# Performance work log

Measured on AMD Instinct MI355X. Metric: run time of the kernel, lower is better.

Reference implementation:

```python
import jax, jax.numpy as jnp
import numpy as np

N = 2048          # num agents / graph nodes
D = 128           # n_actor == n_map
ALPHA = 0.2       # GAT leakyrelu alpha
NEG = -1e9
X_IDX = [4, 9, 14, 19]   # actors_inter_cat time indices per LSTM step
E_IDX = [0, 4, 9, 14]    # graph_adjs time indices per LSTM step


def setup_inputs() -> dict:
    key = jax.random.key(0)
    ks = jax.random.split(key, 10)
    xavier = lambda k, shape: jax.random.uniform(
        k, shape, jnp.float32, -1.0, 1.0) * 1.414 * np.sqrt(6.0 / (shape[-2] + shape[-1]))
    actors_inter_cat = jax.random.normal(ks[0], (N, 20, D), jnp.float32)
    graph_adjs = jax.random.randint(ks[1], (N, 20, N), 0, 2, jnp.int32)
    # 4 GAT_SRF gates (forget, input, input_cell, output), stacked on leading axis
    Wg = xavier(ks[2], (4, 2 * D, D))          # gate projection W: in=2*D, out=D
    ag = xavier(ks[3], (4, 2 * D))             # attention vector a (2*out_features,)
    W = xavier(ks[4], (D, D))                  # GAT cell output projection
    b = xavier(ks[5], (1, D))
    h0 = xavier(ks[6], (1, D))
    conv_w = jax.random.normal(ks[7], (3, D, D, 2), jnp.float32) * (1.0 / np.sqrt(2 * D))
    conv_b = jax.random.normal(ks[8], (3, D), jnp.float32) * 0.01
    return {"actors_inter_cat": actors_inter_cat, "graph_adjs": graph_adjs,
            "Wg": Wg, "ag": ag, "W": W, "b": b, "h0": h0,
            "conv_w": conv_w, "conv_b": conv_b}


def _gat_gates(gin, mask, Wg, ag):
    # gin: (N, 2D); mask: (N, N) bool. Computes all 4 GAT_SRF gates at once.
    Wh = jnp.einsum('nf,gfo->gno', gin, Wg)                 # (4, N, D)
    s_src = jnp.einsum('gno,go->gn', Wh, ag[:, :D])         # a^T [Wh_i ..]
    s_dst = jnp.einsum('gno,go->gn', Wh, ag[:, D:])
    e = jax.nn.leaky_relu(s_src[:, :, None] + s_dst[:, None, :], ALPHA)  # (4,N,N)
    e = jnp.where(mask[None], e, NEG)
    attn = jax.nn.softmax(e, axis=-1)
    return jax.nn.elu(jnp.einsum('gnm,gmo->gno', attn, Wh))  # concat=True -> ELU


def reference(actors_inter_cat, graph_adjs, Wg, ag, W, b, h0, conv_w, conv_b):
    n = actors_inter_cat.shape[0]
    cell = actors_inter_cat[:, 0, :]
    hidden = jnp.broadcast_to(h0, (n, D))
    outs = []
    for t in range(4):  # fixed 4-step recurrence
        X = actors_inter_cat[:, X_IDX[t], :]
        mask = graph_adjs[:, E_IDX[t], :] > 0
        gin = jnp.concatenate([X, hidden], axis=1)          # (N, 2D)
        g = _gat_gates(gin, mask, Wg, ag)                   # (4, N, D)
        forget = jax.nn.sigmoid(g[0])
        inp_gate = jax.nn.sigmoid(g[1])
        inp_cell = jnp.tanh(g[2])
        out_gate = jax.nn.sigmoid(g[3])
        cell = cell * forget + inp_gate * inp_cell
        hidden = jnp.tanh(cell) * out_gate
        outs.append(jax.nn.sigmoid(hidden @ W + b))
    y = jnp.stack(outs, axis=2)                             # (N, D, 4)
    for l in range(3):  # kernel-2 Conv1d stack: length 4 -> 3 -> 2 -> 1
        y = (jnp.einsum('nct,oc->not', y[:, :, :-1], conv_w[l, :, :, 0])
             + jnp.einsum('nct,oc->not', y[:, :, 1:], conv_w[l, :, :, 1])
             + conv_b[l][None, :, None])
    return y[:, :, 0]                                       # squeeze -> (N, D)
```

## Files before the change

kernel.cpp:

```cpp
#include <hip/hip_runtime.h>

typedef __attribute__((ext_vector_type(8))) short short8;
typedef __attribute__((ext_vector_type(4))) float floatx4;

#define MFMA16(a,b,c) __builtin_amdgcn_mfma_f32_16x16x32_bf16(a,b,c,0,0,0)

__device__ __forceinline__ unsigned short f2bf(float f){
  unsigned u = __float_as_uint(f);
  u += 0x7fffu + ((u >> 16) & 1u);
  return (unsigned short)(u >> 16);
}
__device__ __forceinline__ float sigm(float x){ return 1.f/(1.f+__expf(-x)); }


__global__ __launch_bounds__(256) void prep_kernel(const float* __restrict__ actors,
    const float* __restrict__ Wg, const float* __restrict__ W, const float* __restrict__ cw,
    const int* __restrict__ adj, float* __restrict__ cell, unsigned short* __restrict__ WgA,
    unsigned short* __restrict__ WoA, float* __restrict__ cwT,
    unsigned long long* __restrict__ bm){
  int bid = blockIdx.x;
  if (bid < 1024){
    int idx = bid*256 + threadIdx.x;
    int n = idx >> 7, c = idx & 127;
    cell[idx] = actors[(size_t)n*2560 + c];
  } else if (bid < 1536){
    int e = (bid-1024)*256 + threadIdx.x;
    int g = e >> 15, o = (e >> 8) & 127, k = e & 255;
    unsigned short v = f2bf(Wg[(size_t)g*32768 + k*128 + o]);
    int off = ((o>>4)*8 + (k>>5))*512 + (((k>>3)&3)*16 + (o&15))*8 + (k&7);
    WgA[(size_t)g*32768 + off] = v;
  } else if (bid < 1728){
    int e = (bid-1536)*256 + threadIdx.x;
    int l = e >> 14, rr = e & 16383, k = rr >> 7, o = rr & 127;
    cwT[(size_t)l*32768 + k*256 + o]       = cw[(size_t)l*32768 + o*256 + k*2];
    cwT[(size_t)l*32768 + k*256 + 128 + o] = cw[(size_t)l*32768 + o*256 + k*2 + 1];
  } else if (bid < 1792){
    int e = (bid-1728)*256 + threadIdx.x;
    int k = e >> 7, o = e & 127;
    unsigned short v = f2bf(W[(size_t)k*128 + o]);
    int off = ((o>>4)*4 + (k>>5))*512 + (((k>>3)&3)*16 + (o&15))*8 + (k&7);
    WoA[off] = v;
  } else {
    const int E[4] = {0,4,9,14};
    int mb = bid - 1792;
    int t = mb & 3, nblk = mb >> 2;
    int wv = threadIdx.x >> 6, lane = threadIdx.x & 63;
    int n = nblk*4 + wv;
    const int* row = adj + (size_t)n*40960 + (size_t)E[t]*2048;
    unsigned long long* outp = bm + ((size_t)t*2048 + n)*32;
    for (int it=0; it<32; ++it){
      unsigned long long bal = __ballot(row[it*64 + lane] > 0);
      if (lane == 0) outp[it] = bal;
    }
  }
}

__global__ __launch_bounds__(512,2) void gatewh_kernel(const float* __restrict__ actors,
    const float* __restrict__ gbuf, float* __restrict__ cell, const float* __restrict__ h0,
    const float* __restrict__ bvec, const unsigned short* __restrict__ WgA,
    const unsigned short* __restrict__ WoA, const float* __restrict__ ag,
    float* __restrict__ y, unsigned short* __restrict__ WhB,
    float* __restrict__ spart, int xoff, int t){
  __shared__ float hl[16][132];
  __shared__ __align__(16) unsigned short ginb[16*264];
  __shared__ float sredS[4][4][16], sredD[4][4][16];
  int bx = blockIdx.x;
  int tile = bx >> 1, ohalf = bx & 1;
  int n0 = tile*16, tid = threadIdx.x;
  int row = tid>>5, q = tid&31;
  {
    int o0 = q*4;
    if (t == 0){
      *(float4*)&hl[row][o0] = *(const float4*)(h0 + o0);
    } else {
      size_t idx = (size_t)(n0+row)*128 + o0;
      float4 ga = *(const float4*)(gbuf+idx);
      float4 gb = *(const float4*)(gbuf+262144+idx);
      float4 gc = *(const float4*)(gbuf+524288+idx);
      float4 gd = *(const float4*)(gbuf+786432+idx);
      float4 cv = *(const float4*)(cell+idx);
      float fg[4]={ga.x,ga.y,ga.z,ga.w}, ig[4]={gb.x,gb.y,gb.z,gb.w};
      float ic[4]={gc.x,gc.y,gc.z,gc.w}, og[4]={gd.x,gd.y,gd.z,gd.w};
      float cc[4]={cv.x,cv.y,cv.z,cv.w};
      float clv[4];
      #pragma unroll
      for (int j=0;j<4;++j){
        clv[j] = cc[j]*sigm(fg[j]) + sigm(ig[j])*tanhf(ic[j]);
        hl[row][o0+j] = tanhf(clv[j])*sigm(og[j]);
      }
      if (ohalf == 0)
        *(float4*)(cell+idx) = (float4){clv[0],clv[1],clv[2],clv[3]};
    }
  }
  __syncthreads();
  if (q < 16){
    const float* ap = actors + (size_t)(n0+row)*2560 + xoff + q*8;
    float4 a = *(const float4*)ap, bb = *(const float4*)(ap+4);
    unsigned short tmp[8] = {f2bf(a.x),f2bf(a.y),f2bf(a.z),f2bf(a.w),
                             f2bf(bb.x),f2bf(bb.y),f2bf(bb.z),f2bf(bb.w)};
    *(uint4*)&ginb[row*264 + q*8] = *(const uint4*)tmp;
  } else {
    int c0 = (q-16)*8;
    unsigned short tmp[8];
    #pragma unroll
    for (int j=0;j<8;++j) tmp[j] = f2bf(hl[row][c0+j]);
    *(uint4*)&ginb[row*264 + 128 + c0] = *(const uint4*)tmp;
  }
  __syncthreads();
  int w = tid>>6, lane = tid&63, quad = lane>>4, l16 = lane&15;
  int m32 = tile>>1, min32 = (tile&1)*16 + l16;
  int qp = min32>>3, jp = min32&7;
  if (t >= 1 && w < 4){
    int o16 = ohalf*4 + w;
    floatx4 acc = {0.f,0.f,0.f,0.f};
    #pragma unroll
    for (int kh=0; kh<4; ++kh){
      short8 bfr = *(const short8*)&ginb[l16*264 + 128 + kh*32 + quad*8];
      short8 a0 = *(const short8*)(WoA + (size_t)((o16*4 + kh)*64 + lane)*8);
      acc = MFMA16(a0, bfr, acc);
    }
    int oc = o16*16 + quad*4;
    float4 bb = *(const float4*)(bvec + oc);
    float4 res = {sigm(acc[0]+bb.x), sigm(acc[1]+bb.y),
                  sigm(acc[2]+bb.z), sigm(acc[3]+bb.w)};
    *(float4*)(y + (size_t)(t-1)*262144 + (size_t)(n0+l16)*128 + oc) = res;
  }
  #pragma unroll
  for (int ci=0; ci<2; ++ci){
    int cidx = w*2 + ci;
    int g = cidx>>2, o16q = cidx&3, o16 = ohalf*4 + o16q;
    floatx4 acc = {0.f,0.f,0.f,0.f};
    const unsigned short* wa = WgA + (size_t)g*32768;
    #pragma unroll
    for (int kh=0; kh<8; ++kh){
      short8 bfr = *(const short8*)&ginb[l16*264 + kh*32 + quad*8];
      short8 a0 = *(const short8*)(wa + (size_t)((o16*8 + kh)*64 + lane)*8);
      acc = MFMA16(a0, bfr, acc);
    }
    float ps = 0.f, pd = 0.f;
    unsigned short* wb = WhB + (size_t)(g*8 + o16)*32768 + m32*512 + qp*128 + jp;
    const float* agp = ag + g*256;
    #pragma unroll
    for (int r=0;r<4;++r){
      int o = o16*16 + quad*4 + r;
      float v = acc[r];
      ps += v*agp[o]; pd += v*agp[128+o];
      wb[(quad*4+r)*8] = f2bf(v);
    }
    ps += __shfl_down(ps,32); ps += __shfl_down(ps,16);
    pd += __shfl_down(pd,32); pd += __shfl_down(pd,16);
    if (lane < 16){ sredS[g][o16q][l16] = ps; sredD[g][o16q][l16] = pd; }
  }
  __syncthreads();
  if (tid < 128){
    int g = tid>>5, which = (tid>>4)&1, n = tid&15;
    float s;
    if (which) s = sredD[g][0][n]+sredD[g][1][n]+sredD[g][2][n]+sredD[g][3][n];
    else       s = sredS[g][0][n]+sredS[g][1][n]+sredS[g][2][n]+sredS[g][3][n];
    spart[(size_t)((ohalf*2 + which)*4 + g)*2048 + n0 + n] = s;
  }
}

__global__ __launch_bounds__(512,2) void attn_kernel(const unsigned char* __restrict__ bmb,
    const unsigned short* __restrict__ WhB, const float* __restrict__ spart,
    float* __restrict__ gout, int t){
  __shared__ __align__(16) unsigned char smem[131072];
  __shared__ float ssum[2048];
  __shared__ float zpart[8][32];
  int bid = blockIdx.x;
  int g = bid & 3, n0 = (bid >> 2)*32;
  int tid = threadIdx.x;
  int w = tid>>6, lane = tid&63, quad = lane>>4, l16 = lane&15;
  const float* sS0 = spart + (size_t)(0 + g)*2048;
  const float* sD0 = spart + (size_t)(4 + g)*2048;
  const float* sS1 = spart + (size_t)(8 + g)*2048;
  const float* sD1 = spart + (size_t)(12 + g)*2048;
  const unsigned short* wb = WhB + (size_t)g*262144;
  const unsigned short* wbw = wb + (size_t)(w*8)*512;

  {
    unsigned char* lp0 = smem + (size_t)w*8192;
    #pragma unroll
    for (int o16=0;o16<8;++o16)
      __builtin_amdgcn_global_load_lds((const void*)(wbw + (size_t)o16*32768 + lane*8),
                                       (void*)(lp0 + o16*1024), 16, 0, 0);
  }
  {
    float4 d0 = *(const float4*)(sD0 + tid*4);
    float4 d1 = *(const float4*)(sD1 + tid*4);
    *(float4*)&ssum[tid*4] = (float4){d0.x+d1.x, d0.y+d1.y, d0.z+d1.z, d0.w+d1.w};
  }
  float srcv0 = sS0[n0 + l16]      + sS1[n0 + l16];
  float srcv1 = sS0[n0 + 16 + l16] + sS1[n0 + 16 + l16];
  const unsigned char* mr0 = bmb + ((size_t)t*2048 + n0 + l16)*256 + w*32;
  const unsigned char* mr1 = mr0 + 16*256;
  uint4 q0 = *(const uint4*)mr0, q1 = *(const uint4*)(mr0+16);
  uint4 r0 = *(const uint4*)mr1, r1 = *(const uint4*)(mr1+16);
  unsigned mwd0[8] = {q0.x,q0.y,q0.z,q0.w, q1.x,q1.y,q1.z,q1.w};
  unsigned mwd1[8] = {r0.x,r0.y,r0.z,r0.w, r1.x,r1.y,r1.z,r1.w};
  float z0 = 0.f, z1 = 0.f;
  floatx4 acc0[8], acc1[8];
  #pragma unroll
  for (int j=0;j<8;++j){ acc0[j] = (floatx4){0.f,0.f,0.f,0.f}; acc1[j] = acc0[j]; }

  #pragma unroll
  for (int c=0; c<8; ++c){
    const int cur = c & 1;
    if (c < 7){
      unsigned char* lp = smem + (size_t)(((c+1)&1)*8 + w)*8192;
      const unsigned short* gsrc = wbw + (size_t)(c+1)*512 + lane*8;
      #pragma unroll
      for (int o16=0;o16<8;++o16)
        __builtin_amdgcn_global_load_lds((const void*)(gsrc + (size_t)o16*32768),
                                         (void*)(lp + o16*1024), 16, 0, 0);
      asm volatile("s_waitcnt vmcnt(8)" ::: "memory");
    } else {
      asm volatile("s_waitcnt vmcnt(0)" ::: "memory");
    }
    __builtin_amdgcn_sched_barrier(0);
    int mk = w*256 + c*32 + quad*8;
    float4 sa = *(const float4*)&ssum[mk];
    float4 sb = *(const float4*)&ssum[mk+4];
    float sv[8] = {sa.x,sa.y,sa.z,sa.w, sb.x,sb.y,sb.z,sb.w};
    unsigned mb0 = (mwd0[c] >> (quad*8)) & 0xffu;
    unsigned mb1 = (mwd1[c] >> (quad*8)) & 0xffu;
    short8 A0, A1;
    #pragma unroll
    for (int j=0;j<8;++j){
      float s0 = srcv0 + sv[j];
      s0 = fmaxf(s0, 0.2f*s0);
      float p0 = ((mb0 >> j) & 1u) ? __expf(s0) : 0.f;
      z0 += p0;
      A0[j] = (short)f2bf(p0);
      float s1 = srcv1 + sv[j];
      s1 = fmaxf(s1, 0.2f*s1);
      float p1 = ((mb1 >> j) & 1u) ? __expf(s1) : 0.f;
      z1 += p1;
      A1[j] = (short)f2bf(p1);
    }
    const unsigned char* sb_base = smem + (size_t)(cur*8 + w)*8192 + lane*16;
    #pragma unroll
    for (int o16=0; o16<8; ++o16){
      short8 bfr = *(const short8*)(sb_base + o16*1024);
      acc0[o16] = MFMA16(A0, bfr, acc0[o16]);
      acc1[o16] = MFMA16(A1, bfr, acc1[o16]);
    }
  }
  z0 += __shfl_down(z0,32); z0 += __shfl_down(z0,16);
  z1 += __shfl_down(z1,32); z1 += __shfl_down(z1,16);
  if (lane < 16){ zpart[w][l16] = z0; zpart[w][16+l16] = z1; }
  __syncthreads();
  float (*obuf)[32][132] = (float (*)[32][132])smem;
  if (w < 4){
    #pragma unroll
    for (int o16=0;o16<8;++o16)
      #pragma unroll
      for (int r=0;r<4;++r){
        obuf[w][quad*4+r][o16*16+l16]      = acc0[o16][r];
        obuf[w][16+quad*4+r][o16*16+l16]   = acc1[o16][r];
      }
  }
  __syncthreads();
  if (w >= 4){
    #pragma unroll
    for (int o16=0;o16<8;++o16)
      #pragma unroll
      for (int r=0;r<4;++r){
        obuf[w-4][quad*4+r][o16*16+l16]    += acc0[o16][r];
        obuf[w-4][16+quad*4+r][o16*16+l16] += acc1[o16][r];
      }
  }
  __syncthreads();
  {
    int row = tid>>4, c0 = (tid&15)*8;
    float z = zpart[0][row]+zpart[1][row]+zpart[2][row]+zpart[3][row]
            + zpart[4][row]+zpart[5][row]+zpart[6][row]+zpart[7][row];
    float inv = 1.f / z;
    float* go = gout + (size_t)g*262144 + (size_t)(n0+row)*128 + c0;
    #pragma unroll
    for (int j=0;j<8;++j){
      float v = (obuf[0][row][c0+j] + obuf[1][row][c0+j]
               + obuf[2][row][c0+j] + obuf[3][row][c0+j]) * inv;
      go[j] = v > 0.f ? v : __expf(v) - 1.f;
    }
  }
}

__global__ __launch_bounds__(256) void convgate_kernel(const float* __restrict__ gbuf,
    const float* __restrict__ cell, const float* __restrict__ W, const float* __restrict__ bvec,
    const float* __restrict__ y, const float* __restrict__ cwT, const float* __restrict__ cb,
    float* __restrict__ out){
  __shared__ float hl[4][128];
  __shared__ float ylds[4][128][4];
  int tid = threadIdx.x;
  int r = tid >> 6, oc = (tid & 63)*2;
  int n = blockIdx.x*4 + r;
  size_t idx = (size_t)n*128 + oc;
  {
    float2 g0 = *(const float2*)(gbuf+idx),        g1 = *(const float2*)(gbuf+262144+idx);
    float2 g2 = *(const float2*)(gbuf+524288+idx), g3 = *(const float2*)(gbuf+786432+idx);
    float2 cv = *(const float2*)(cell+idx);
    float fg[2]={g0.x,g0.y}, ig[2]={g1.x,g1.y}, ic[2]={g2.x,g2.y}, og[2]={g3.x,g3.y};
    float cc[2]={cv.x,cv.y};
    #pragma unroll
    for (int j=0;j<2;++j){
      float cl = cc[j]*sigm(fg[j]) + sigm(ig[j])*tanhf(ic[j]);
      hl[r][oc+j] = tanhf(cl)*sigm(og[j]);
    }
  }
  {
    float2 y0 = *(const float2*)(y+idx), y1 = *(const float2*)(y+262144+idx),
           y2 = *(const float2*)(y+524288+idx);
    float a0[2]={y0.x,y0.y}, a1[2]={y1.x,y1.y}, a2[2]={y2.x,y2.y};
    #pragma unroll
    for (int j=0;j<2;++j){
      ylds[r][oc+j][0]=a0[j]; ylds[r][oc+j][1]=a1[j]; ylds[r][oc+j][2]=a2[j];
    }
  }
  __syncthreads();
  {
    float2 bb = *(const float2*)(bvec+oc);
    float acc[2] = {bb.x, bb.y};
    const float* hr = hl[r];
    for (int k=0;k<128;++k){
      float hv = hr[k];
      float2 wv = *(const float2*)(W + (size_t)k*128 + oc);
      acc[0]+=hv*wv.x; acc[1]+=hv*wv.y;
    }
    #pragma unroll
    for (int j=0;j<2;++j) ylds[r][oc+j][3] = sigm(acc[j]);
  }
  __syncthreads();
  {
    float a0[2]={0,0}, a1[2]={0,0}, a2[2]={0,0};
    for (int k=0;k<128;++k){
      float2 w0 = *(const float2*)(cwT + k*256 + oc);
      float2 w1 = *(const float2*)(cwT + k*256 + 128 + oc);
      float4 yv = *(const float4*)&ylds[r][k][0];
      float wa[2]={w0.x,w0.y}, wb2[2]={w1.x,w1.y};
      #pragma unroll
      for (int j=0;j<2;++j){
        a0[j] += yv.x*wa[j] + yv.y*wb2[j];
        a1[j] += yv.y*wa[j] + yv.z*wb2[j];
        a2[j] += yv.z*wa[j] + yv.w*wb2[j];
      }
    }
    float2 bb = *(const float2*)(cb+oc);
    float bbv[2]={bb.x,bb.y};
    __syncthreads();
    #pragma unroll
    for (int j=0;j<2;++j){
      ylds[r][oc+j][0]=a0[j]+bbv[j]; ylds[r][oc+j][1]=a1[j]+bbv[j]; ylds[r][oc+j][2]=a2[j]+bbv[j];
    }
    __syncthreads();
  }
  {
    float a0[2]={0,0}, a1[2]={0,0};
    for (int k=0;k<128;++k){
      float2 w0 = *(const float2*)(cwT + 32768 + k*256 + oc);
      float2 w1 = *(const float2*)(cwT + 32768 + k*256 + 128 + oc);
      float4 yv = *(const float4*)&ylds[r][k][0];
      float wa[2]={w0.x,w0.y}, wb2[2]={w1.x,w1.y};
      #pragma unroll
      for (int j=0;j<2;++j){
        a0[j] += yv.x*wa[j] + yv.y*wb2[j];
        a1[j] += yv.y*wa[j] + yv.z*wb2[j];
      }
    }
    float2 bb = *(const float2*)(cb+128+oc);
    float bbv[2]={bb.x,bb.y};
    __syncthreads();
    #pragma unroll
    for (int j=0;j<2;++j){
      ylds[r][oc+j][0]=a0[j]+bbv[j]; ylds[r][oc+j][1]=a1[j]+bbv[j];
    }
    __syncthreads();
  }
  {
    float a0[2]={0,0};
    for (int k=0;k<128;++k){
      float2 w0 = *(const float2*)(cwT + 65536 + k*256 + oc);
      float2 w1 = *(const float2*)(cwT + 65536 + k*256 + 128 + oc);
      float4 yv = *(const float4*)&ylds[r][k][0];
      a0[0] += yv.x*w0.x + yv.y*w1.x;
      a0[1] += yv.x*w0.y + yv.y*w1.y;
    }
    float2 bb = *(const float2*)(cb+256+oc);
    float2 res = {a0[0]+bb.x, a0[1]+bb.y};
    *(float2*)(out+idx) = res;
  }
}

extern "C" void kernel_launch(void* const* d_in, const int* in_sizes, int n_in,
                              void* d_out, int out_size, void* d_ws, size_t ws_size,
                              hipStream_t stream) {
  const float* actors = (const float*)d_in[0];
  const int*   adj    = (const int*)d_in[1];
  const float* Wg     = (const float*)d_in[2];
  const float* ag     = (const float*)d_in[3];
  const float* W      = (const float*)d_in[4];
  const float* b      = (const float*)d_in[5];
  const float* h0     = (const float*)d_in[6];
  const float* cw     = (const float*)d_in[7];
  const float* cb     = (const float*)d_in[8];
  float* out = (float*)d_out;

  char* ws = (char*)d_ws;
  unsigned long long* bm = (unsigned long long*)ws;
  float* cell          = (float*)(ws + (size_t)(2u<<20));
  unsigned short* WgA  = (unsigned short*)(ws + (size_t)(3u<<20));
  float* cwT           = (float*)(ws + (size_t)3407872);
  unsigned short* WoA  = (unsigned short*)(ws + (size_t)3801088);
  float* spart         = (float*)(ws + (size_t)3932160);
  unsigned short* WhB  = (unsigned short*)(ws + (size_t)(4u<<20));
  float* gbuf          = (float*)(ws + (size_t)(7u<<20));
  float* yplanes       = (float*)(ws + (size_t)(11u<<20));

  const int XI[4] = {4, 9, 14, 19};

  prep_kernel<<<3840, 256, 0, stream>>>(actors, Wg, W, cw, adj, cell, WgA, WoA, cwT, bm);
  for (int t=0; t<4; ++t){
    gatewh_kernel<<<256, 512, 0, stream>>>(actors, gbuf, cell, h0, b, WgA, WoA, ag,
                                           yplanes, WhB, spart, XI[t]*128, t);
    attn_kernel<<<256, 512, 0, stream>>>((const unsigned char*)bm, WhB,
                                         spart, gbuf, t);
  }
  convgate_kernel<<<512, 256, 0, stream>>>(gbuf, cell, W, b, yplanes, cwT, cb, out);
}
```

Measured before the change: 562.6 us.

## Retile attention kernel to 64 rows by 64 output columns, pack bf16 conversion

The attention kernel now gives each block 64 rows and half of the 128 output columns (4x4 MFMA tiles per wave) instead of 32 rows by all 128 columns. Each loaded Wh B-fragment is reused across four row groups, and LDS use per block shrinks by about half, which may allow higher occupancy. The exp/mask work per row is now done twice, once per column half, and bf16 packing uses v_cvt_pk_bf16_f32. tanhf is also replaced by an exp-based fast tanh in the gate kernels, which may slightly change precision for large inputs.

```diff
diff --git a/kernel.cpp b/kernel.cpp
--- a/kernel.cpp
+++ b/kernel.cpp
@@ -10,7 +10,16 @@
   u += 0x7fffu + ((u >> 16) & 1u);
   return (unsigned short)(u >> 16);
 }
+__device__ __forceinline__ unsigned cvtpk(float lo, float hi){
+  unsigned r;
+  asm("v_cvt_pk_bf16_f32 %0, %1, %2" : "=v"(r) : "v"(lo), "v"(hi));
+  return r;
+}
 __device__ __forceinline__ float sigm(float x){ return 1.f/(1.f+__expf(-x)); }
+__device__ __forceinline__ float tanh_fast(float x){
+  float e = __expf(2.f*x);
+  return 1.f - 2.f/(e+1.f);
+}
 
 
 __global__ __launch_bounds__(256) void prep_kernel(const float* __restrict__ actors,
@@ -85,8 +94,8 @@
       float clv[4];
       #pragma unroll
       for (int j=0;j<4;++j){
-        clv[j] = cc[j]*sigm(fg[j]) + sigm(ig[j])*tanhf(ic[j]);
-        hl[row][o0+j] = tanhf(clv[j])*sigm(og[j]);
+        clv[j] = cc[j]*sigm(fg[j]) + sigm(ig[j])*tanh_fast(ic[j]);
+        hl[row][o0+j] = tanh_fast(clv[j])*sigm(og[j]);
       }
       if (ohalf == 0)
         *(float4*)(cell+idx) = (float4){clv[0],clv[1],clv[2],clv[3]};
@@ -164,56 +173,65 @@
 __global__ __launch_bounds__(512,2) void attn_kernel(const unsigned char* __restrict__ bmb,
     const unsigned short* __restrict__ WhB, const float* __restrict__ spart,
     float* __restrict__ gout, int t){
-  __shared__ __align__(16) unsigned char smem[131072];
+  __shared__ __align__(16) unsigned char smem[67584];
   __shared__ float ssum[2048];
-  __shared__ float zpart[8][32];
+  __shared__ float zpart[8][64];
   int bid = blockIdx.x;
-  int g = bid & 3, n0 = (bid >> 2)*32;
+  int g = bid & 3, rb = bid >> 2;
+  int rowblk = rb >> 1, ohalf = rb & 1;
+  int n0 = rowblk*64;
   int tid = threadIdx.x;
   int w = tid>>6, lane = tid&63, quad = lane>>4, l16 = lane&15;
   const float* sS0 = spart + (size_t)(0 + g)*2048;
   const float* sD0 = spart + (size_t)(4 + g)*2048;
   const float* sS1 = spart + (size_t)(8 + g)*2048;
   const float* sD1 = spart + (size_t)(12 + g)*2048;
-  const unsigned short* wb = WhB + (size_t)g*262144;
-  const unsigned short* wbw = wb + (size_t)(w*8)*512;
-
-  {
-    unsigned char* lp0 = smem + (size_t)w*8192;
-    #pragma unroll
-    for (int o16=0;o16<8;++o16)
-      __builtin_amdgcn_global_load_lds((const void*)(wbw + (size_t)o16*32768 + lane*8),
-                                       (void*)(lp0 + o16*1024), 16, 0, 0);
+  const unsigned short* wb0 = WhB + (size_t)(g*8 + ohalf*4)*32768;
+
+  unsigned mwd[4][8];
+  #pragma unroll
+  for (int rg=0; rg<4; ++rg){
+    const unsigned char* mr = bmb + ((size_t)t*2048 + n0 + rg*16 + l16)*256 + w*32;
+    uint4 a = *(const uint4*)mr, b = *(const uint4*)(mr+16);
+    mwd[rg][0]=a.x; mwd[rg][1]=a.y; mwd[rg][2]=a.z; mwd[rg][3]=a.w;
+    mwd[rg][4]=b.x; mwd[rg][5]=b.y; mwd[rg][6]=b.z; mwd[rg][7]=b.w;
+  }
+  float srcv[4];
+  #pragma unroll
+  for (int rg=0; rg<4; ++rg)
+    srcv[rg] = sS0[n0 + rg*16 + l16] + sS1[n0 + rg*16 + l16];
+
+  {
+    unsigned char* lp = smem + (size_t)w*4096;
+    const unsigned short* gs = wb0 + (size_t)(w*8)*512 + lane*8;
+    #pragma unroll
+    for (int oq=0; oq<4; ++oq)
+      __builtin_amdgcn_global_load_lds((const void*)(gs + (size_t)oq*32768),
+                                       (void*)(lp + oq*1024), 16, 0, 0);
   }
   {
     float4 d0 = *(const float4*)(sD0 + tid*4);
     float4 d1 = *(const float4*)(sD1 + tid*4);
     *(float4*)&ssum[tid*4] = (float4){d0.x+d1.x, d0.y+d1.y, d0.z+d1.z, d0.w+d1.w};
   }
-  float srcv0 = sS0[n0 + l16]      + sS1[n0 + l16];
-  float srcv1 = sS0[n0 + 16 + l16] + sS1[n0 + 16 + l16];
-  const unsigned char* mr0 = bmb + ((size_t)t*2048 + n0 + l16)*256 + w*32;
-  const unsigned char* mr1 = mr0 + 16*256;
-  uint4 q0 = *(const uint4*)mr0, q1 = *(const uint4*)(mr0+16);
-  uint4 r0 = *(const uint4*)mr1, r1 = *(const uint4*)(mr1+16);
-  unsigned mwd0[8] = {q0.x,q0.y,q0.z,q0.w, q1.x,q1.y,q1.z,q1.w};
-  unsigned mwd1[8] = {r0.x,r0.y,r0.z,r0.w, r1.x,r1.y,r1.z,r1.w};
-  float z0 = 0.f, z1 = 0.f;
-  floatx4 acc0[8], acc1[8];
-  #pragma unroll
-  for (int j=0;j<8;++j){ acc0[j] = (floatx4){0.f,0.f,0.f,0.f}; acc1[j] = acc0[j]; }
+  float z[4] = {0.f,0.f,0.f,0.f};
+  floatx4 acc[4][4];
+  #pragma unroll
+  for (int rg=0;rg<4;++rg)
+    #pragma unroll
+    for (int oq=0;oq<4;++oq) acc[rg][oq] = (floatx4){0.f,0.f,0.f,0.f};
 
   #pragma unroll
   for (int c=0; c<8; ++c){
     const int cur = c & 1;
     if (c < 7){
-      unsigned char* lp = smem + (size_t)(((c+1)&1)*8 + w)*8192;
-      const unsigned short* gsrc = wbw + (size_t)(c+1)*512 + lane*8;
-      #pragma unroll
-      for (int o16=0;o16<8;++o16)
-        __builtin_amdgcn_global_load_lds((const void*)(gsrc + (size_t)o16*32768),
-                                         (void*)(lp + o16*1024), 16, 0, 0);
-      asm volatile("s_waitcnt vmcnt(8)" ::: "memory");
+      unsigned char* lp = smem + (size_t)(((c+1)&1)*8 + w)*4096;
+      const unsigned short* gs = wb0 + (size_t)(w*8 + c + 1)*512 + lane*8;
+      #pragma unroll
+      for (int oq=0; oq<4; ++oq)
+        __builtin_amdgcn_global_load_lds((const void*)(gs + (size_t)oq*32768),
+                                         (void*)(lp + oq*1024), 16, 0, 0);
+      asm volatile("s_waitcnt vmcnt(4)" ::: "memory");
     } else {
       asm volatile("s_waitcnt vmcnt(0)" ::: "memory");
     }
@@ -222,61 +240,66 @@
     float4 sa = *(const float4*)&ssum[mk];
     float4 sb = *(const float4*)&ssum[mk+4];
     float sv[8] = {sa.x,sa.y,sa.z,sa.w, sb.x,sb.y,sb.z,sb.w};
-    unsigned mb0 = (mwd0[c] >> (quad*8)) & 0xffu;
-    unsigned mb1 = (mwd1[c] >> (quad*8)) & 0xffu;
-    short8 A0, A1;
-    #pragma unroll
-    for (int j=0;j<8;++j){
-      float s0 = srcv0 + sv[j];
-      s0 = fmaxf(s0, 0.2f*s0);
-      float p0 = ((mb0 >> j) & 1u) ? __expf(s0) : 0.f;
-      z0 += p0;
-      A0[j] = (short)f2bf(p0);
-      float s1 = srcv1 + sv[j];
-      s1 = fmaxf(s1, 0.2f*s1);
-      float p1 = ((mb1 >> j) & 1u) ? __expf(s1) : 0.f;
-      z1 += p1;
-      A1[j] = (short)f2bf(p1);
-    }
-    const unsigned char* sb_base = smem + (size_t)(cur*8 + w)*8192 + lane*16;
-    #pragma unroll
-    for (int o16=0; o16<8; ++o16){
-      short8 bfr = *(const short8*)(sb_base + o16*1024);
-      acc0[o16] = MFMA16(A0, bfr, acc0[o16]);
-      acc1[o16] = MFMA16(A1, bfr, acc1[o16]);
-    }
-  }
-  z0 += __shfl_down(z0,32); z0 += __shfl_down(z0,16);
-  z1 += __shfl_down(z1,32); z1 += __shfl_down(z1,16);
-  if (lane < 16){ zpart[w][l16] = z0; zpart[w][16+l16] = z1; }
-  __syncthreads();
-  float (*obuf)[32][132] = (float (*)[32][132])smem;
+    short8 bfr[4];
+    const unsigned char* sbase = smem + (size_t)(cur*8 + w)*4096 + lane*16;
+    #pragma unroll
+    for (int oq=0; oq<4; ++oq) bfr[oq] = *(const short8*)(sbase + oq*1024);
+    #pragma unroll
+    for (int rg=0; rg<4; ++rg){
+      unsigned mb = (mwd[rg][c] >> (quad*8)) & 0xffu;
+      float p[8];
+      #pragma unroll
+      for (int j=0;j<8;++j){
+        float s = srcv[rg] + sv[j];
+        s = fmaxf(s, 0.2f*s);
+        p[j] = ((mb >> j) & 1u) ? __expf(s) : 0.f;
+        z[rg] += p[j];
+      }
+      union { short8 v; unsigned u[4]; } A;
+      #pragma unroll
+      for (int j2=0;j2<4;++j2) A.u[j2] = cvtpk(p[2*j2], p[2*j2+1]);
+      #pragma unroll
+      for (int oq=0; oq<4; ++oq)
+        acc[rg][oq] = MFMA16(A.v, bfr[oq], acc[rg][oq]);
+    }
+  }
+  #pragma unroll
+  for (int rg=0; rg<4; ++rg){
+    z[rg] += __shfl_down(z[rg],32);
+    z[rg] += __shfl_down(z[rg],16);
+  }
+  if (lane < 16){
+    #pragma unroll
+    for (int rg=0; rg<4; ++rg) zpart[w][rg*16+l16] = z[rg];
+  }
+  __syncthreads();
+  float (*obuf)[64][66] = (float (*)[64][66])smem;
   if (w < 4){
     #pragma unroll
-    for (int o16=0;o16<8;++o16)
-      #pragma unroll
-      for (int r=0;r<4;++r){
-        obuf[w][quad*4+r][o16*16+l16]      = acc0[o16][r];
-        obuf[w][16+quad*4+r][o16*16+l16]   = acc1[o16][r];
-      }
+    for (int rg=0; rg<4; ++rg)
+      #pragma unroll
+      for (int oq=0; oq<4; ++oq)
+        #pragma unroll
+        for (int r=0; r<4; ++r)
+          obuf[w][rg*16+quad*4+r][oq*16+l16] = acc[rg][oq][r];
   }
   __syncthreads();
   if (w >= 4){
     #pragma unroll
-    for (int o16=0;o16<8;++o16)
-      #pragma unroll
-      for (int r=0;r<4;++r){
-        obuf[w-4][quad*4+r][o16*16+l16]    += acc0[o16][r];
-        obuf[w-4][16+quad*4+r][o16*16+l16] += acc1[o16][r];
-      }
-  }
-  __syncthreads();
-  {
-    int row = tid>>4, c0 = (tid&15)*8;
-    float z = zpart[0][row]+zpart[1][row]+zpart[2][row]+zpart[3][row]
-            + zpart[4][row]+zpart[5][row]+zpart[6][row]+zpart[7][row];
-    float inv = 1.f / z;
-    float* go = gout + (size_t)g*262144 + (size_t)(n0+row)*128 + c0;
+    for (int rg=0; rg<4; ++rg)
+      #pragma unroll
+      for (int oq=0; oq<4; ++oq)
+        #pragma unroll
+        for (int r=0; r<4; ++r)
+          obuf[w-4][rg*16+quad*4+r][oq*16+l16] += acc[rg][oq][r];
+  }
+  __syncthreads();
+  {
+    int row = tid>>3, c0 = (tid&7)*8;
+    float zz = zpart[0][row]+zpart[1][row]+zpart[2][row]+zpart[3][row]
+             + zpart[4][row]+zpart[5][row]+zpart[6][row]+zpart[7][row];
+    float inv = 1.f / zz;
+    float* go = gout + (size_t)g*262144 + (size_t)(n0+row)*128 + ohalf*64 + c0;
     #pragma unroll
     for (int j=0;j<8;++j){
       float v = (obuf[0][row][c0+j] + obuf[1][row][c0+j]
@@ -304,8 +327,8 @@
     float cc[2]={cv.x,cv.y};
     #pragma unroll
     for (int j=0;j<2;++j){
-      float cl = cc[j]*sigm(fg[j]) + sigm(ig[j])*tanhf(ic[j]);
-      hl[r][oc+j] = tanhf(cl)*sigm(og[j]);
+      float cl = cc[j]*sigm(fg[j]) + sigm(ig[j])*tanh_fast(ic[j]);
+      hl[r][oc+j] = tanh_fast(cl)*sigm(og[j]);
     }
   }
   {
```

New measurement: 574.1 us. 1.02x slower.
